# Kernel optimization log

Hardware: AMD Instinct MI355X
Metric: run time of the kernel (lower is better)

The kernel has to match this reference:

```python
import jax, jax.numpy as jnp
import numpy as np

B, T, H, K = 128, 512, 1024, 7
START, STOP = 5, 6
NEG = -10000.0


def setup_inputs() -> dict:
    key = jax.random.key(0)
    k1, k2, k3, k4, k5, k6 = jax.random.split(key, 6)
    features = jax.random.normal(k1, (B, T, H), dtype=jnp.float32)
    tags = jax.random.randint(k2, (B, T), 0, 5, dtype=jnp.int32)  # BIESO only
    lengths = jax.random.randint(k3, (B,), 1, T + 1, dtype=jnp.int32)
    W = jax.random.normal(k4, (K, H), dtype=jnp.float32) * (1.0 / np.sqrt(H))
    b = jax.random.normal(k5, (K,), dtype=jnp.float32) * 0.01
    transitions = jax.random.normal(k6, (K, K), dtype=jnp.float32)
    transitions = transitions.at[START, :].set(NEG)  # nothing transitions into START
    transitions = transitions.at[:, STOP].set(NEG)   # nothing transitions out of STOP
    return {"features": features, "tags": tags, "lengths": lengths,
            "W": W, "b": b, "transitions": transitions}


def _crf_loss(features, W, b, transitions, tags, lengths):
    feats = jnp.einsum('bth,kh->btk', features, W) + b  # [B,T,K] emissions
    Bn, Tn, Kn = feats.shape

    # ---- forward algorithm (partition function) ----
    init = jnp.full((Bn, Kn), NEG, dtype=feats.dtype).at[:, START].set(0.0)

    def step(fv, inp):
        emit, i = inp  # emit: [B,K]
        # tag_var[b, next, prev] = emit[b, next] + trans[next, prev] + fv[b, prev]
        tv = emit[:, :, None] + transitions[None, :, :] + fv[:, None, :]
        new = jax.nn.logsumexp(tv, axis=2)  # [B,K]
        fv = jnp.where((i < lengths)[:, None], new, fv)  # freeze past sentence end
        return fv, None

    fv, _ = jax.lax.scan(step, init, (jnp.swapaxes(feats, 0, 1), jnp.arange(Tn)))
    terminal = fv + transitions[STOP][None, :]
    forward_score = jax.nn.logsumexp(terminal, axis=1)  # [B]

    # ---- gold score ----
    pad_start = jnp.concatenate(
        [jnp.full((Bn, 1), START, tags.dtype), tags], axis=1)  # [B,T+1]
    pad_stop = jnp.concatenate(
        [tags, jnp.full((Bn, 1), STOP, tags.dtype)], axis=1)   # [B,T+1]
    j = jnp.arange(Tn + 1)[None, :]
    pad_stop = jnp.where(j >= lengths[:, None], STOP, pad_stop)
    trans_sc = jnp.sum(
        jnp.where(j <= lengths[:, None], transitions[pad_stop, pad_start], 0.0),
        axis=1)
    t = jnp.arange(Tn)[None, :]
    emit_sel = jnp.take_along_axis(feats, tags[:, :, None].astype(jnp.int32), axis=2)[:, :, 0]
    emit_sc = jnp.sum(jnp.where(t < lengths[:, None], emit_sel, 0.0), axis=1)
    gold_score = trans_sc + emit_sc  # [B]

    return jnp.sum(forward_score - gold_score)


def reference(features, tags, lengths, W, b, transitions):
    return _crf_loss(features, W, b, transitions, tags, lengths)
```

## Files before the change

### kernel.cpp

```cpp
#include <hip/hip_runtime.h>

#define B_ 128
#define T_ 512
#define H_ 1024
#define K_ 7
#define START_ 5
#define STOP_ 6
#define LOG2E 1.4426950408889634f
#define LN2 0.6931471805599453f
#define NEG2 (-10000.0f * 1.4426950408889634f)
#define MS 57

typedef float f32x4 __attribute__((ext_vector_type(4)));

__device__ __forceinline__ float fexp2(float x) { return __builtin_amdgcn_exp2f(x); }
__device__ __forceinline__ float flog2(float x) { return __builtin_amdgcn_logf(x); }
__device__ __forceinline__ f32x4 ntload(const float* p) {
  return __builtin_nontemporal_load((const f32x4*)p);
}

#define COMPUTE_ROW(R0, R1, R2, R3, CUR)                                        \
  do {                                                                          \
    float acc[8];                                                               \
    _Pragma("unroll") for (int k = 0; k < 8; ++k) acc[k] = 0.0f;                \
    _Pragma("unroll") for (int k = 0; k < K_; ++k) {                            \
      acc[k] += R0.x * w[k][0].x + R0.y * w[k][0].y + R0.z * w[k][0].z + R0.w * w[k][0].w; \
      acc[k] += R1.x * w[k][1].x + R1.y * w[k][1].y + R1.z * w[k][1].z + R1.w * w[k][1].w; \
      acc[k] += R2.x * w[k][2].x + R2.y * w[k][2].y + R2.z * w[k][2].z + R2.w * w[k][2].w; \
      acc[k] += R3.x * w[k][3].x + R3.y * w[k][3].y + R3.z * w[k][3].z + R3.w * w[k][3].w; \
    }                                                                           \
    const bool b0 = lane & 1;                                                   \
    float k0 = b0 ? acc[4] : acc[0], s0 = b0 ? acc[0] : acc[4];                 \
    float k1 = b0 ? acc[5] : acc[1], s1 = b0 ? acc[1] : acc[5];                 \
    float k2 = b0 ? acc[6] : acc[2], s2 = b0 ? acc[2] : acc[6];                 \
    float k3 = b0 ? acc[7] : acc[3], s3 = b0 ? acc[3] : acc[7];                 \
    k0 += __shfl_xor(s0, 1, 64); k1 += __shfl_xor(s1, 1, 64);                   \
    k2 += __shfl_xor(s2, 1, 64); k3 += __shfl_xor(s3, 1, 64);                   \
    const bool b1 = lane & 2;                                                   \
    float m0 = b1 ? k2 : k0, t0 = b1 ? k0 : k2;                                 \
    float m1 = b1 ? k3 : k1, t1 = b1 ? k1 : k3;                                 \
    m0 += __shfl_xor(t0, 2, 64); m1 += __shfl_xor(t1, 2, 64);                   \
    const bool b2 = lane & 4;                                                   \
    float x = b2 ? m1 : m0, y = b2 ? m0 : m1;                                   \
    x += __shfl_xor(y, 4, 64);                                                  \
    x += __shfl_xor(x, 8, 64);                                                  \
    x += __shfl_xor(x, 16, 64);                                                 \
    x += __shfl_xor(x, 32, 64);                                                 \
    if (lane < 8 && vidx < K_)                                                  \
      e2[(size_t)(CUR) * 8 + vidx] = (x + myb) * LOG2E;                         \
  } while (0)

#define LOAD_ROW(R0, R1, R2, R3, J)                                             \
  do {                                                                          \
    const float* p_ = features + (size_t)(gwave + (J) * NW) * H_ + lane * 4;    \
    R0 = ntload(p_); R1 = ntload(p_ + 256);                                     \
    R2 = ntload(p_ + 512); R3 = ntload(p_ + 768);                               \
  } while (0)

__global__ __launch_bounds__(256, 2) void emis_kernel(
    const float* __restrict__ features, const float* __restrict__ W,
    const float* __restrict__ bias, float* __restrict__ e2, float* __restrict__ out) {
  if (blockIdx.x == 0 && threadIdx.x == 0) out[0] = 0.0f;

  const int tid = threadIdx.x;
  const int lane = tid & 63;
  const int gwave = blockIdx.x * 4 + (tid >> 6);
  const int NW = 2048;

  f32x4 w[K_][4];
#pragma unroll
  for (int k = 0; k < K_; ++k)
#pragma unroll
    for (int c = 0; c < 4; ++c)
      w[k][c] = *(const f32x4*)(W + k * H_ + c * 256 + lane * 4);

  const int vidx = ((lane & 1) << 2) | (lane & 2) | ((lane >> 2) & 1);
  float myb = 0.0f;
  if (vidx < K_) myb = bias[vidx];

  f32x4 A0, A1, A2, A3, B0, B1, B2, B3, C0, C1, C2, C3;
  LOAD_ROW(A0, A1, A2, A3, 0);
  LOAD_ROW(B0, B1, B2, B3, 1);
  LOAD_ROW(C0, C1, C2, C3, 2);

  for (int jj = 0; jj < 9; ++jj) {
    const int j0 = 3 * jj;
    COMPUTE_ROW(A0, A1, A2, A3, gwave + j0 * NW);
    LOAD_ROW(A0, A1, A2, A3, j0 + 3);
    COMPUTE_ROW(B0, B1, B2, B3, gwave + (j0 + 1) * NW);
    LOAD_ROW(B0, B1, B2, B3, j0 + 4);
    COMPUTE_ROW(C0, C1, C2, C3, gwave + (j0 + 2) * NW);
    LOAD_ROW(C0, C1, C2, C3, j0 + 5);
  }
  COMPUTE_ROW(A0, A1, A2, A3, gwave + 27 * NW);
  LOAD_ROW(A0, A1, A2, A3, 30);
  COMPUTE_ROW(B0, B1, B2, B3, gwave + 28 * NW);
  LOAD_ROW(B0, B1, B2, B3, 31);
  COMPUTE_ROW(C0, C1, C2, C3, gwave + 29 * NW);
  COMPUTE_ROW(A0, A1, A2, A3, gwave + 30 * NW);
  COMPUTE_ROW(B0, B1, B2, B3, gwave + 31 * NW);
}

template <int NM>
__device__ __forceinline__ void level_fn(const float* __restrict__ evenB,
                                         const float* __restrict__ oddB,
                                         int qstride, float* __restrict__ dst,
                                         int tid) {
  constexpr int TOT = NM * 49;
  constexpr int NI = (TOT + 511) / 512;
  float tmp[NI];
#pragma unroll
  for (int i = 0; i < NI; ++i) {
    const int u = tid + i * 512;
    if (u < TOT) {
      const int q = u / 49, r = u - 49 * q, n = r / 7, p = r - 7 * n;
      const float* hi = oddB + q * qstride;
      const float* lo = evenB + q * qstride;
      float qq[7];
#pragma unroll
      for (int m = 0; m < 7; ++m) qq[m] = hi[n * 8 + m] + lo[m * 8 + p];
      float mx = fmaxf(fmaxf(fmaxf(qq[0], qq[1]), fmaxf(qq[2], qq[3])),
                       fmaxf(fmaxf(qq[4], qq[5]), qq[6]));
      float s = 0.f;
#pragma unroll
      for (int m = 0; m < 7; ++m) s += fexp2(qq[m] - mx);
      tmp[i] = mx + flog2(s);
    }
  }
  __syncthreads();
#pragma unroll
  for (int i = 0; i < NI; ++i) {
    const int u = tid + i * 512;
    if (u < TOT) {
      const int q = u / 49, r = u - 49 * q, n = r / 7, p = r - 7 * n;
      dst[q * MS + n * 8 + p] = tmp[i];
    }
  }
  __syncthreads();
}

__global__ __launch_bounds__(512) void scan_kernel(
    const float* __restrict__ e2, const int* __restrict__ tags,
    const int* __restrict__ lengths, const float* __restrict__ transitions,
    float* __restrict__ out) {
  __shared__ float s0[128 * MS];
  __shared__ float s1[128 * MS];
  __shared__ float tr2s[49];
  __shared__ float red[4];

  const int tid = threadIdx.x;
  const int b = blockIdx.x;
  const int len = lengths[b];

  if (tid < 49) tr2s[tid] = transitions[tid] * LOG2E;
  __syncthreads();

  const int* tg = tags + (size_t)b * T_;
  const float* ep = e2 + (size_t)b * T_ * 8;

  if (tid < 256) {
    const int t0 = 2 * tid, t1 = 2 * tid + 1;
    float P[7][7];
    if (t1 < len) {
      const f32x4* ev = (const f32x4*)(ep + (size_t)t0 * 8);
      const f32x4 ca = ev[0], cb = ev[1], da = ev[2], db = ev[3];
      const float c[7]  = {ca.x, ca.y, ca.z, ca.w, cb.x, cb.y, cb.z};
      const float e1[7] = {da.x, da.y, da.z, da.w, db.x, db.y, db.z};
#pragma unroll
      for (int n = 0; n < 7; ++n) {
        float a[7];
#pragma unroll
        for (int m = 0; m < 7; ++m) a[m] = tr2s[n * 7 + m] + c[m];
#pragma unroll
        for (int p = 0; p < 7; ++p) {
          float s = 1e-37f;
#pragma unroll
          for (int m = 0; m < 7; ++m) s += fexp2(a[m] + tr2s[m * 7 + p]);
          P[n][p] = e1[n] + flog2(s);
        }
      }
    } else if (t0 < len) {
      const f32x4* ev = (const f32x4*)(ep + (size_t)t0 * 8);
      const f32x4 ca = ev[0], cb = ev[1];
      const float c[7] = {ca.x, ca.y, ca.z, ca.w, cb.x, cb.y, cb.z};
#pragma unroll
      for (int n = 0; n < 7; ++n) {
#pragma unroll
        for (int p = 0; p < 7; ++p) P[n][p] = c[n] + tr2s[n * 7 + p];
      }
    } else {
#pragma unroll
      for (int n = 0; n < 7; ++n)
#pragma unroll
        for (int p = 0; p < 7; ++p) P[n][p] = (n == p) ? 0.f : NEG2;
    }
    float* dstm = ((tid & 1) ? s1 : s0) + (tid >> 1) * MS;
#pragma unroll
    for (int n = 0; n < 7; ++n)
#pragma unroll
      for (int p = 0; p < 7; ++p) dstm[n * 8 + p] = P[n][p];
  } else {
    const int t2 = tid - 256;
    float gp = 0.f;
    for (int t = t2; t < len; t += 256) {
      const int tag = tg[t];
      const int prev = t ? tg[t - 1] : START_;
      gp += ep[(size_t)t * 8 + tag] + tr2s[tag * 7 + prev];
    }
#pragma unroll
    for (int off = 32; off; off >>= 1) gp += __shfl_xor(gp, off, 64);
    if ((tid & 63) == 0) red[(tid >> 6) - 4] = gp;
  }
  __syncthreads();

  level_fn<128>(s0, s1, MS, s0, tid);
  level_fn<64>(s0, s0 + MS, 2 * MS, s1, tid);
  level_fn<32>(s1, s1 + MS, 2 * MS, s0, tid);
  level_fn<16>(s0, s0 + MS, 2 * MS, s1, tid);
  level_fn<8>(s1, s1 + MS, 2 * MS, s0, tid);
  level_fn<4>(s0, s0 + MS, 2 * MS, s1, tid);
  level_fn<2>(s1, s1 + MS, 2 * MS, s0, tid);
  level_fn<1>(s0, s0 + MS, 2 * MS, s1, tid);

  if (tid == 0) {
    float tt[7];
#pragma unroll
    for (int n = 0; n < 7; ++n) tt[n] = s1[n * 8 + START_] + tr2s[STOP_ * 7 + n];
    float mx = tt[0];
#pragma unroll
    for (int n = 1; n < 7; ++n) mx = fmaxf(mx, tt[n]);
    float s = 0.f;
#pragma unroll
    for (int n = 0; n < 7; ++n) s += fexp2(tt[n] - mx);
    const float fwd = mx + flog2(s);
    const float gold = red[0] + red[1] + red[2] + red[3] +
                       tr2s[STOP_ * 7 + tg[len - 1]];
    atomicAdd(out, (fwd - gold) * LN2);
  }
}

extern "C" void kernel_launch(void* const* d_in, const int* in_sizes, int n_in,
                              void* d_out, int out_size, void* d_ws, size_t ws_size,
                              hipStream_t stream) {
  const float* features    = (const float*)d_in[0];
  const int*   tags        = (const int*)d_in[1];
  const int*   lengths     = (const int*)d_in[2];
  const float* W           = (const float*)d_in[3];
  const float* bias        = (const float*)d_in[4];
  const float* transitions = (const float*)d_in[5];
  float* out = (float*)d_out;
  float* e2  = (float*)d_ws;

  emis_kernel<<<512, 256, 0, stream>>>(features, W, bias, e2, out);
  scan_kernel<<<B_, 512, 0, stream>>>(e2, tags, lengths, transitions, out);
}
```

Before: 59.96 us.

## Fuse emission GEMV with per-chunk CRF matrix scan, add small combine kernel

The emission projection and the log-semiring tree scan are merged into one kernel. Each block handles a 128-step chunk of one sequence, keeps its emissions in shared memory, and reduces the chunk to a 7x7 transfer matrix plus a partial gold score. A small combine kernel then merges the four chunk matrices per sequence. This removes the global round-trip of emissions and the serial 8-level scan on only 128 blocks. The cost is a second launch, and the heavy scan phase now sits after the bandwidth-bound feature reads inside each block, so the two may no longer overlap well.

```diff
diff --git a/kernel.cpp b/kernel.cpp
--- a/kernel.cpp
+++ b/kernel.cpp
@@ -10,6 +10,9 @@
 #define LN2 0.6931471805599453f
 #define NEG2 (-10000.0f * 1.4426950408889634f)
 #define MS 57
+#define CHUNK 128
+#define NCHUNK (B_ * T_ / CHUNK)
+#define CWS 64
 
 typedef float f32x4 __attribute__((ext_vector_type(4)));
 
@@ -19,7 +22,7 @@
   return __builtin_nontemporal_load((const f32x4*)p);
 }
 
-#define COMPUTE_ROW(R0, R1, R2, R3, CUR)                                        \
+#define COMPUTE_ROW(R0, R1, R2, R3, LR)                                         \
   do {                                                                          \
     float acc[8];                                                               \
     _Pragma("unroll") for (int k = 0; k < 8; ++k) acc[k] = 0.0f;                \
@@ -30,88 +33,43 @@
       acc[k] += R3.x * w[k][3].x + R3.y * w[k][3].y + R3.z * w[k][3].z + R3.w * w[k][3].w; \
     }                                                                           \
     const bool b0 = lane & 1;                                                   \
-    float k0 = b0 ? acc[4] : acc[0], s0 = b0 ? acc[0] : acc[4];                 \
-    float k1 = b0 ? acc[5] : acc[1], s1 = b0 ? acc[1] : acc[5];                 \
-    float k2 = b0 ? acc[6] : acc[2], s2 = b0 ? acc[2] : acc[6];                 \
-    float k3 = b0 ? acc[7] : acc[3], s3 = b0 ? acc[3] : acc[7];                 \
-    k0 += __shfl_xor(s0, 1, 64); k1 += __shfl_xor(s1, 1, 64);                   \
-    k2 += __shfl_xor(s2, 1, 64); k3 += __shfl_xor(s3, 1, 64);                   \
+    float k0 = b0 ? acc[4] : acc[0], s0_ = b0 ? acc[0] : acc[4];                \
+    float k1 = b0 ? acc[5] : acc[1], s1_ = b0 ? acc[1] : acc[5];                \
+    float k2 = b0 ? acc[6] : acc[2], s2_ = b0 ? acc[2] : acc[6];                \
+    float k3 = b0 ? acc[7] : acc[3], s3_ = b0 ? acc[3] : acc[7];                \
+    k0 += __shfl_xor(s0_, 1, 64); k1 += __shfl_xor(s1_, 1, 64);                 \
+    k2 += __shfl_xor(s2_, 1, 64); k3 += __shfl_xor(s3_, 1, 64);                 \
     const bool b1 = lane & 2;                                                   \
-    float m0 = b1 ? k2 : k0, t0 = b1 ? k0 : k2;                                 \
-    float m1 = b1 ? k3 : k1, t1 = b1 ? k1 : k3;                                 \
-    m0 += __shfl_xor(t0, 2, 64); m1 += __shfl_xor(t1, 2, 64);                   \
+    float m0 = b1 ? k2 : k0, t0_ = b1 ? k0 : k2;                                \
+    float m1 = b1 ? k3 : k1, t1_ = b1 ? k1 : k3;                                \
+    m0 += __shfl_xor(t0_, 2, 64); m1 += __shfl_xor(t1_, 2, 64);                 \
     const bool b2 = lane & 4;                                                   \
     float x = b2 ? m1 : m0, y = b2 ? m0 : m1;                                   \
     x += __shfl_xor(y, 4, 64);                                                  \
     x += __shfl_xor(x, 8, 64);                                                  \
     x += __shfl_xor(x, 16, 64);                                                 \
     x += __shfl_xor(x, 32, 64);                                                 \
-    if (lane < 8 && vidx < K_)                                                  \
-      e2[(size_t)(CUR) * 8 + vidx] = (x + myb) * LOG2E;                         \
+    if (lane < 8 && vidx < K_) ech[LR][vidx] = (x + myb) * LOG2E;               \
   } while (0)
 
 #define LOAD_ROW(R0, R1, R2, R3, J)                                             \
   do {                                                                          \
-    const float* p_ = features + (size_t)(gwave + (J) * NW) * H_ + lane * 4;    \
+    const float* p_ = features + (rowbase + (size_t)(J)) * H_ + lane * 4;       \
     R0 = ntload(p_); R1 = ntload(p_ + 256);                                     \
     R2 = ntload(p_ + 512); R3 = ntload(p_ + 768);                               \
   } while (0)
 
-__global__ __launch_bounds__(256, 2) void emis_kernel(
-    const float* __restrict__ features, const float* __restrict__ W,
-    const float* __restrict__ bias, float* __restrict__ e2, float* __restrict__ out) {
-  if (blockIdx.x == 0 && threadIdx.x == 0) out[0] = 0.0f;
-
-  const int tid = threadIdx.x;
-  const int lane = tid & 63;
-  const int gwave = blockIdx.x * 4 + (tid >> 6);
-  const int NW = 2048;
-
-  f32x4 w[K_][4];
-#pragma unroll
-  for (int k = 0; k < K_; ++k)
-#pragma unroll
-    for (int c = 0; c < 4; ++c)
-      w[k][c] = *(const f32x4*)(W + k * H_ + c * 256 + lane * 4);
-
-  const int vidx = ((lane & 1) << 2) | (lane & 2) | ((lane >> 2) & 1);
-  float myb = 0.0f;
-  if (vidx < K_) myb = bias[vidx];
-
-  f32x4 A0, A1, A2, A3, B0, B1, B2, B3, C0, C1, C2, C3;
-  LOAD_ROW(A0, A1, A2, A3, 0);
-  LOAD_ROW(B0, B1, B2, B3, 1);
-  LOAD_ROW(C0, C1, C2, C3, 2);
-
-  for (int jj = 0; jj < 9; ++jj) {
-    const int j0 = 3 * jj;
-    COMPUTE_ROW(A0, A1, A2, A3, gwave + j0 * NW);
-    LOAD_ROW(A0, A1, A2, A3, j0 + 3);
-    COMPUTE_ROW(B0, B1, B2, B3, gwave + (j0 + 1) * NW);
-    LOAD_ROW(B0, B1, B2, B3, j0 + 4);
-    COMPUTE_ROW(C0, C1, C2, C3, gwave + (j0 + 2) * NW);
-    LOAD_ROW(C0, C1, C2, C3, j0 + 5);
-  }
-  COMPUTE_ROW(A0, A1, A2, A3, gwave + 27 * NW);
-  LOAD_ROW(A0, A1, A2, A3, 30);
-  COMPUTE_ROW(B0, B1, B2, B3, gwave + 28 * NW);
-  LOAD_ROW(B0, B1, B2, B3, 31);
-  COMPUTE_ROW(C0, C1, C2, C3, gwave + 29 * NW);
-  COMPUTE_ROW(A0, A1, A2, A3, gwave + 30 * NW);
-  COMPUTE_ROW(B0, B1, B2, B3, gwave + 31 * NW);
-}
-
 template <int NM>
-__device__ __forceinline__ void level_fn(const float* __restrict__ evenB,
+__device__ __forceinline__ void level256(const float* __restrict__ evenB,
                                          const float* __restrict__ oddB,
                                          int qstride, float* __restrict__ dst,
                                          int tid) {
   constexpr int TOT = NM * 49;
-  constexpr int NI = (TOT + 511) / 512;
+  constexpr int NI = (TOT + 255) / 256;
   float tmp[NI];
 #pragma unroll
   for (int i = 0; i < NI; ++i) {
-    const int u = tid + i * 512;
+    const int u = tid + i * 256;
     if (u < TOT) {
       const int q = u / 49, r = u - 49 * q, n = r / 7, p = r - 7 * n;
       const float* hi = oddB + q * qstride;
@@ -130,7 +88,7 @@
   __syncthreads();
 #pragma unroll
   for (int i = 0; i < NI; ++i) {
-    const int u = tid + i * 512;
+    const int u = tid + i * 256;
     if (u < TOT) {
       const int q = u / 49, r = u - 49 * q, n = r / 7, p = r - 7 * n;
       dst[q * MS + n * 8 + p] = tmp[i];
@@ -139,102 +97,180 @@
   __syncthreads();
 }
 
-__global__ __launch_bounds__(512) void scan_kernel(
-    const float* __restrict__ e2, const int* __restrict__ tags,
+__global__ __launch_bounds__(256, 2) void fused_kernel(
+    const float* __restrict__ features, const float* __restrict__ W,
+    const float* __restrict__ bias, const int* __restrict__ tags,
+    const int* __restrict__ lengths, const float* __restrict__ transitions,
+    float* __restrict__ cws, float* __restrict__ out) {
+  if (blockIdx.x == 0 && threadIdx.x == 0) out[0] = 0.0f;
+
+  __shared__ float ech[CHUNK][8];
+  __shared__ float s0[32 * MS];
+  __shared__ float s1[32 * MS];
+  __shared__ float tr2s[49];
+  __shared__ float gred[2];
+
+  const int tid = threadIdx.x;
+  const int lane = tid & 63;
+  const int wv = tid >> 6;
+  const int chunk = blockIdx.x;
+  const int b = chunk >> 2;
+  const int cs = (chunk & 3) * CHUNK;
+  const int len = lengths[b];
+  const size_t rowbase = (size_t)b * T_ + cs + wv * 32;
+
+  if (tid < 49) tr2s[tid] = transitions[tid] * LOG2E;
+
+  f32x4 w[K_][4];
+#pragma unroll
+  for (int k = 0; k < K_; ++k)
+#pragma unroll
+    for (int c = 0; c < 4; ++c)
+      w[k][c] = *(const f32x4*)(W + k * H_ + c * 256 + lane * 4);
+
+  const int vidx = ((lane & 1) << 2) | (lane & 2) | ((lane >> 2) & 1);
+  float myb = 0.0f;
+  if (vidx < K_) myb = bias[vidx];
+
+  f32x4 A0, A1, A2, A3, B0, B1, B2, B3, C0, C1, C2, C3;
+  LOAD_ROW(A0, A1, A2, A3, 0);
+  LOAD_ROW(B0, B1, B2, B3, 1);
+  LOAD_ROW(C0, C1, C2, C3, 2);
+
+  for (int jj = 0; jj < 9; ++jj) {
+    const int j0 = 3 * jj;
+    COMPUTE_ROW(A0, A1, A2, A3, wv * 32 + j0);
+    LOAD_ROW(A0, A1, A2, A3, j0 + 3);
+    COMPUTE_ROW(B0, B1, B2, B3, wv * 32 + j0 + 1);
+    LOAD_ROW(B0, B1, B2, B3, j0 + 4);
+    COMPUTE_ROW(C0, C1, C2, C3, wv * 32 + j0 + 2);
+    LOAD_ROW(C0, C1, C2, C3, j0 + 5);
+  }
+  COMPUTE_ROW(A0, A1, A2, A3, wv * 32 + 27);
+  LOAD_ROW(A0, A1, A2, A3, 30);
+  COMPUTE_ROW(B0, B1, B2, B3, wv * 32 + 28);
+  LOAD_ROW(B0, B1, B2, B3, 31);
+  COMPUTE_ROW(C0, C1, C2, C3, wv * 32 + 29);
+  COMPUTE_ROW(A0, A1, A2, A3, wv * 32 + 30);
+  COMPUTE_ROW(B0, B1, B2, B3, wv * 32 + 31);
+  __syncthreads();
+
+  const int* tg = tags + (size_t)b * T_;
+  if (tid < CHUNK) {
+    const int tglob = cs + tid;
+    float gp = 0.f;
+    if (tglob < len) {
+      const int tag = tg[tglob];
+      const int prev = tglob ? tg[tglob - 1] : START_;
+      gp = ech[tid][tag] + tr2s[tag * 7 + prev];
+    }
+#pragma unroll
+    for (int off = 32; off; off >>= 1) gp += __shfl_xor(gp, off, 64);
+    if (lane == 0) gred[wv] = gp;
+  }
+
+  {
+    constexpr int TOT = 64 * 49;
+    constexpr int NI = (TOT + 255) / 256;
+#pragma unroll
+    for (int i = 0; i < NI; ++i) {
+      const int u = tid + i * 256;
+      if (u < TOT) {
+        const int q = u / 49, r = u - 49 * q, n = r / 7, p = r - 7 * n;
+        const int lt0 = 2 * q, t0 = cs + lt0;
+        float val;
+        if (t0 + 1 < len) {
+          float s = 1e-37f;
+#pragma unroll
+          for (int m = 0; m < 7; ++m)
+            s += fexp2(tr2s[n * 7 + m] + ech[lt0][m] + tr2s[m * 7 + p]);
+          val = ech[lt0 + 1][n] + flog2(s);
+        } else if (t0 < len) {
+          val = ech[lt0][n] + tr2s[n * 7 + p];
+        } else {
+          val = (n == p) ? 0.f : NEG2;
+        }
+        float* dstm = ((q & 1) ? s1 : s0) + (q >> 1) * MS;
+        dstm[n * 8 + p] = val;
+      }
+    }
+  }
+  __syncthreads();
+
+  level256<32>(s0, s1, MS, s0, tid);
+  level256<16>(s0, s0 + MS, 2 * MS, s1, tid);
+  level256<8>(s1, s1 + MS, 2 * MS, s0, tid);
+  level256<4>(s0, s0 + MS, 2 * MS, s1, tid);
+  level256<2>(s1, s1 + MS, 2 * MS, s0, tid);
+  level256<1>(s0, s0 + MS, 2 * MS, s1, tid);
+
+  float* cw = cws + (size_t)chunk * CWS;
+  if (tid < 49) cw[tid] = s1[(tid / 7) * 8 + (tid % 7)];
+  if (tid == 49 + 0) cw[49] = gred[0] + gred[1];
+}
+
+__global__ __launch_bounds__(64) void combine_kernel(
+    const float* __restrict__ cws, const int* __restrict__ tags,
     const int* __restrict__ lengths, const float* __restrict__ transitions,
     float* __restrict__ out) {
-  __shared__ float s0[128 * MS];
-  __shared__ float s1[128 * MS];
-  __shared__ float tr2s[49];
-  __shared__ float red[4];
-
+  __shared__ float m01[49], m23[49], fin[49];
   const int tid = threadIdx.x;
   const int b = blockIdx.x;
-  const int len = lengths[b];
-
-  if (tid < 49) tr2s[tid] = transitions[tid] * LOG2E;
-  __syncthreads();
-
-  const int* tg = tags + (size_t)b * T_;
-  const float* ep = e2 + (size_t)b * T_ * 8;
-
-  if (tid < 256) {
-    const int t0 = 2 * tid, t1 = 2 * tid + 1;
-    float P[7][7];
-    if (t1 < len) {
-      const f32x4* ev = (const f32x4*)(ep + (size_t)t0 * 8);
-      const f32x4 ca = ev[0], cb = ev[1], da = ev[2], db = ev[3];
-      const float c[7]  = {ca.x, ca.y, ca.z, ca.w, cb.x, cb.y, cb.z};
-      const float e1[7] = {da.x, da.y, da.z, da.w, db.x, db.y, db.z};
-#pragma unroll
-      for (int n = 0; n < 7; ++n) {
-        float a[7];
-#pragma unroll
-        for (int m = 0; m < 7; ++m) a[m] = tr2s[n * 7 + m] + c[m];
-#pragma unroll
-        for (int p = 0; p < 7; ++p) {
-          float s = 1e-37f;
-#pragma unroll
-          for (int m = 0; m < 7; ++m) s += fexp2(a[m] + tr2s[m * 7 + p]);
-          P[n][p] = e1[n] + flog2(s);
-        }
-      }
-    } else if (t0 < len) {
-      const f32x4* ev = (const f32x4*)(ep + (size_t)t0 * 8);
-      const f32x4 ca = ev[0], cb = ev[1];
-      const float c[7] = {ca.x, ca.y, ca.z, ca.w, cb.x, cb.y, cb.z};
-#pragma unroll
-      for (int n = 0; n < 7; ++n) {
-#pragma unroll
-        for (int p = 0; p < 7; ++p) P[n][p] = c[n] + tr2s[n * 7 + p];
-      }
-    } else {
-#pragma unroll
-      for (int n = 0; n < 7; ++n)
-#pragma unroll
-        for (int p = 0; p < 7; ++p) P[n][p] = (n == p) ? 0.f : NEG2;
-    }
-    float* dstm = ((tid & 1) ? s1 : s0) + (tid >> 1) * MS;
-#pragma unroll
-    for (int n = 0; n < 7; ++n)
-#pragma unroll
-      for (int p = 0; p < 7; ++p) dstm[n * 8 + p] = P[n][p];
-  } else {
-    const int t2 = tid - 256;
-    float gp = 0.f;
-    for (int t = t2; t < len; t += 256) {
-      const int tag = tg[t];
-      const int prev = t ? tg[t - 1] : START_;
-      gp += ep[(size_t)t * 8 + tag] + tr2s[tag * 7 + prev];
-    }
-#pragma unroll
-    for (int off = 32; off; off >>= 1) gp += __shfl_xor(gp, off, 64);
-    if ((tid & 63) == 0) red[(tid >> 6) - 4] = gp;
-  }
-  __syncthreads();
-
-  level_fn<128>(s0, s1, MS, s0, tid);
-  level_fn<64>(s0, s0 + MS, 2 * MS, s1, tid);
-  level_fn<32>(s1, s1 + MS, 2 * MS, s0, tid);
-  level_fn<16>(s0, s0 + MS, 2 * MS, s1, tid);
-  level_fn<8>(s1, s1 + MS, 2 * MS, s0, tid);
-  level_fn<4>(s0, s0 + MS, 2 * MS, s1, tid);
-  level_fn<2>(s1, s1 + MS, 2 * MS, s0, tid);
-  level_fn<1>(s0, s0 + MS, 2 * MS, s1, tid);
+  const float* base = cws + (size_t)b * 4 * CWS;
+  const float* M0 = base;
+  const float* M1 = base + CWS;
+  const float* M2 = base + 2 * CWS;
+  const float* M3 = base + 3 * CWS;
+
+  const int n = tid / 7, p = tid % 7;
+  if (tid < 49) {
+    float qq[7], mx, s;
+#pragma unroll
+    for (int m = 0; m < 7; ++m) qq[m] = M1[n * 7 + m] + M0[m * 7 + p];
+    mx = fmaxf(fmaxf(fmaxf(qq[0], qq[1]), fmaxf(qq[2], qq[3])),
+               fmaxf(fmaxf(qq[4], qq[5]), qq[6]));
+    s = 0.f;
+#pragma unroll
+    for (int m = 0; m < 7; ++m) s += fexp2(qq[m] - mx);
+    m01[tid] = mx + flog2(s);
+#pragma unroll
+    for (int m = 0; m < 7; ++m) qq[m] = M3[n * 7 + m] + M2[m * 7 + p];
+    mx = fmaxf(fmaxf(fmaxf(qq[0], qq[1]), fmaxf(qq[2], qq[3])),
+               fmaxf(fmaxf(qq[4], qq[5]), qq[6]));
+    s = 0.f;
+#pragma unroll
+    for (int m = 0; m < 7; ++m) s += fexp2(qq[m] - mx);
+    m23[tid] = mx + flog2(s);
+  }
+  __syncthreads();
+  if (tid < 49) {
+    float qq[7];
+#pragma unroll
+    for (int m = 0; m < 7; ++m) qq[m] = m23[n * 7 + m] + m01[m * 7 + p];
+    float mx = fmaxf(fmaxf(fmaxf(qq[0], qq[1]), fmaxf(qq[2], qq[3])),
+                     fmaxf(fmaxf(qq[4], qq[5]), qq[6]));
+    float s = 0.f;
+#pragma unroll
+    for (int m = 0; m < 7; ++m) s += fexp2(qq[m] - mx);
+    fin[tid] = mx + flog2(s);
+  }
+  __syncthreads();
 
   if (tid == 0) {
+    const int len = lengths[b];
     float tt[7];
 #pragma unroll
-    for (int n = 0; n < 7; ++n) tt[n] = s1[n * 8 + START_] + tr2s[STOP_ * 7 + n];
+    for (int nn = 0; nn < 7; ++nn)
+      tt[nn] = fin[nn * 7 + START_] + transitions[STOP_ * 7 + nn] * LOG2E;
     float mx = tt[0];
 #pragma unroll
-    for (int n = 1; n < 7; ++n) mx = fmaxf(mx, tt[n]);
+    for (int nn = 1; nn < 7; ++nn) mx = fmaxf(mx, tt[nn]);
     float s = 0.f;
 #pragma unroll
-    for (int n = 0; n < 7; ++n) s += fexp2(tt[n] - mx);
+    for (int nn = 0; nn < 7; ++nn) s += fexp2(tt[nn] - mx);
     const float fwd = mx + flog2(s);
-    const float gold = red[0] + red[1] + red[2] + red[3] +
-                       tr2s[STOP_ * 7 + tg[len - 1]];
+    const float gold = M0[49] + M1[49] + M2[49] + M3[49] +
+                       transitions[STOP_ * 7 + tags[(size_t)b * T_ + len - 1]] * LOG2E;
     atomicAdd(out, (fwd - gold) * LN2);
   }
 }
@@ -249,8 +285,9 @@
   const float* bias        = (const float*)d_in[4];
   const float* transitions = (const float*)d_in[5];
   float* out = (float*)d_out;
-  float* e2  = (float*)d_ws;
-
-  emis_kernel<<<512, 256, 0, stream>>>(features, W, bias, e2, out);
-  scan_kernel<<<B_, 512, 0, stream>>>(e2, tags, lengths, transitions, out);
-}
+  float* cws = (float*)d_ws;
+
+  fused_kernel<<<NCHUNK, 256, 0, stream>>>(features, W, bias, tags, lengths,
+                                           transitions, cws, out);
+  combine_kernel<<<B_, 64, 0, stream>>>(cws, tags, lengths, transitions, out);
+}
```

Result: no change. 60.16 us (+0.3%).
